# Kernel tuning notes

Measured on AMD Instinct MI355X. Metric: run time of the kernel, lower is better.

Reference implementation:

```python
import jax, jax.numpy as jnp
import numpy as np

B, S, D_MODEL, D_QK, D_VO = 4, 2048, 1024, 128, 128
NEG = -1.0e9


def setup_inputs() -> dict:
    key = jax.random.key(0)
    k1, k2, k3, k4, k5 = jax.random.split(key, 5)
    enc = jax.random.normal(k1, (B, S, D_MODEL), dtype=jnp.float32)
    # causal mask: True means masked (masked_fill), broadcast over batch
    causal = jnp.triu(jnp.ones((S, S), dtype=bool), k=1)
    mask = jnp.broadcast_to(causal, (B, S, S))
    scale = 0.02
    W_q = jax.random.normal(k2, (D_MODEL, D_QK), dtype=jnp.float32) * scale
    W_k = jax.random.normal(k3, (D_MODEL, D_QK), dtype=jnp.float32) * scale
    W_v = jax.random.normal(k4, (D_MODEL, D_VO), dtype=jnp.float32) * scale
    W_o = jax.random.normal(k5, (D_VO, D_MODEL), dtype=jnp.float32) * scale
    return {"encodings": enc, "mask": mask, "W_q": W_q, "W_k": W_k, "W_v": W_v, "W_o": W_o}


def reference(encodings, mask, W_q, W_k, W_v, W_o):
    # q,k: [B,S,d_qk]; v: [B,S,d_vo]
    q = jnp.einsum('bsd,de->bse', encodings, W_q)
    k = jnp.einsum('bsd,de->bse', encodings, W_k)
    v = jnp.einsum('bsd,de->bse', encodings, W_v)
    sims = jnp.einsum('bqe,bke->bqk', q, k) / jnp.asarray(D_QK ** 0.5, q.dtype)
    sims = jnp.where(mask, jnp.asarray(NEG, sims.dtype), sims)
    attn = jax.nn.softmax(sims, axis=-1)  # [B,S,S]
    scores = jnp.einsum('bqk,bke->bqe', attn, v)  # [B,S,d_vo]
    return jnp.einsum('bse,ed->bsd', scores, W_o)  # [B,S,d_model]
```

## Files before the change

kernel.cpp:

```cpp
#include <hip/hip_runtime.h>
#include <hip/hip_bf16.h>
#include <stdint.h>

typedef __attribute__((ext_vector_type(8))) short short8;
typedef __attribute__((ext_vector_type(4))) float floatx4;

using bf16 = __hip_bfloat16;

#define SCALE_L2 0.12751793359133147f

__device__ inline unsigned short f2b(float f) {
    bf16 h = __float2bfloat16(f);
    return *(unsigned short*)&h;
}
__device__ inline float b2f(unsigned short u) {
    union { unsigned int i; float f; } v;
    v.i = ((unsigned int)u) << 16;
    return v.f;
}

__device__ __forceinline__ void gll16(const bf16* g, bf16* l) {
    __builtin_amdgcn_global_load_lds((__attribute__((address_space(1))) void*)g,
                                     (__attribute__((address_space(3))) void*)l,
                                     16, 0, 0);
}

__global__ __launch_bounds__(256) void prep_w(const float* __restrict__ Wq,
                                              const float* __restrict__ Wk,
                                              const float* __restrict__ Wv,
                                              const float* __restrict__ Wo,
                                              bf16* __restrict__ Wqkvt,
                                              bf16* __restrict__ Wot) {
    int idx = blockIdx.x * 256 + threadIdx.x;
    int sel = idx >> 17;
    int i = idx & 131071;
    if (sel < 3) {
        const float* W = (sel == 0) ? Wq : (sel == 1) ? Wk : Wv;
        int r = i >> 7, c = i & 127;
        Wqkvt[(size_t)(sel * 128 + c) * 1024 + r] = __float2bfloat16(W[i]);
    } else {
        int r = i >> 10, c = i & 1023;
        Wot[(size_t)c * 128 + r] = __float2bfloat16(Wo[i]);
    }
}

__global__ __launch_bounds__(256) void gemm_qkv(const float* __restrict__ enc,
                                                const bf16* __restrict__ Bt,
                                                bf16* __restrict__ Qb,
                                                bf16* __restrict__ Kb,
                                                bf16* __restrict__ Vtb) {
    __shared__ __align__(16) bf16 As[32 * 32];
    __shared__ __align__(16) bf16 Bs[128 * 32];

    const int tid = threadIdx.x;
    const int m0 = blockIdx.x * 32;
    const int nsel = blockIdx.y;
    const int brow0 = nsel * 128;
    const int w = tid >> 6, lane = tid & 63;
    const int wr = (w >> 1) * 16, wc = (w & 1) * 64;
    const int quad = lane >> 4, l16 = lane & 15;

    const int ar = tid >> 3, af = tid & 7;
    const int br = w * 16 + (lane >> 2), bk = (lane & 3) * 8;

    const float4* Arow4 = (const float4*)&enc[(size_t)(m0 + ar) * 1024];
    float4 a0 = Arow4[af];

    floatx4 acc[4];
#pragma unroll
    for (int j = 0; j < 4; j++) acc[j] = (floatx4){0.f, 0.f, 0.f, 0.f};

    for (int k0 = 0; k0 < 1024; k0 += 32) {
        __syncthreads();
        gll16(&Bt[(size_t)(brow0 + br) * 1024 + k0 + bk], &Bs[w * 512]);
        gll16(&Bt[(size_t)(brow0 + 64 + br) * 1024 + k0 + bk], &Bs[2048 + w * 512]);
        ushort4 u0;
        u0.x = f2b(a0.x); u0.y = f2b(a0.y); u0.z = f2b(a0.z); u0.w = f2b(a0.w);
        *(ushort4*)&As[ar * 32 + af * 4] = u0;
        __syncthreads();

        if (k0 + 32 < 1024)
            a0 = Arow4[((k0 + 32) >> 2) + af];

        short8 a = *(const short8*)&As[(wr + l16) * 32 + quad * 8];
        short8 bfr[4];
#pragma unroll
        for (int nt = 0; nt < 4; nt++)
            bfr[nt] = *(const short8*)&Bs[(wc + nt * 16 + l16) * 32 + quad * 8];
#pragma unroll
        for (int nt = 0; nt < 4; nt++)
            acc[nt] = __builtin_amdgcn_mfma_f32_16x16x32_bf16(a, bfr[nt], acc[nt], 0, 0, 0);
    }

#pragma unroll
    for (int nt = 0; nt < 4; nt++)
#pragma unroll
        for (int r = 0; r < 4; r++) {
            int row = m0 + wr + quad * 4 + r;
            int col = wc + nt * 16 + l16;
            bf16 h = __float2bfloat16(acc[nt][r]);
            if (nsel == 0) {
                Qb[(size_t)row * 128 + col] = h;
            } else if (nsel == 1) {
                Kb[(size_t)row * 128 + col] = h;
            } else {
                int bb = row >> 11, ss = row & 2047;
                Vtb[(size_t)bb * 262144 + (size_t)col * 2048 + ss] = h;
            }
        }
}

__global__ __launch_bounds__(256) void gemm_out(const bf16* __restrict__ A,
                                                const bf16* __restrict__ Bt,
                                                float* __restrict__ C) {
    __shared__ bf16 As[64 * 40];
    __shared__ bf16 Bs[128 * 40];

    const int tid = threadIdx.x;
    const int m0 = blockIdx.x * 64;
    const int n0 = blockIdx.y * 128;
    const int w = tid >> 6, lane = tid & 63;
    const int wm = (w >> 1) * 32, wn = (w & 1) * 64;
    const int quad = lane >> 4, l16 = lane & 15;

    const int ra = tid >> 2, ca = (tid & 3) * 8;
    const int rb0 = tid >> 2, rb1 = (tid + 256) >> 2;

    floatx4 acc[2][4];
#pragma unroll
    for (int i = 0; i < 2; i++)
#pragma unroll
        for (int j = 0; j < 4; j++) acc[i][j] = (floatx4){0.f, 0.f, 0.f, 0.f};

    int4 pa  = *(const int4*)&A[(size_t)(m0 + ra) * 128 + ca];
    int4 pb0 = *(const int4*)&Bt[(size_t)(n0 + rb0) * 128 + ca];
    int4 pb1 = *(const int4*)&Bt[(size_t)(n0 + rb1) * 128 + ca];

    for (int k0 = 0; k0 < 128; k0 += 32) {
        __syncthreads();
        *(int4*)&As[ra * 40 + ca] = pa;
        *(int4*)&Bs[rb0 * 40 + ca] = pb0;
        *(int4*)&Bs[rb1 * 40 + ca] = pb1;
        __syncthreads();

        if (k0 + 32 < 128) {
            pa  = *(const int4*)&A[(size_t)(m0 + ra) * 128 + k0 + 32 + ca];
            pb0 = *(const int4*)&Bt[(size_t)(n0 + rb0) * 128 + k0 + 32 + ca];
            pb1 = *(const int4*)&Bt[(size_t)(n0 + rb1) * 128 + k0 + 32 + ca];
        }

        short8 a[2], b[4];
#pragma unroll
        for (int mt = 0; mt < 2; mt++)
            a[mt] = *(const short8*)&As[(wm + mt * 16 + l16) * 40 + quad * 8];
#pragma unroll
        for (int nt = 0; nt < 4; nt++)
            b[nt] = *(const short8*)&Bs[(wn + nt * 16 + l16) * 40 + quad * 8];
#pragma unroll
        for (int mt = 0; mt < 2; mt++)
#pragma unroll
            for (int nt = 0; nt < 4; nt++)
                acc[mt][nt] = __builtin_amdgcn_mfma_f32_16x16x32_bf16(a[mt], b[nt], acc[mt][nt], 0, 0, 0);
    }

#pragma unroll
    for (int mt = 0; mt < 2; mt++)
#pragma unroll
        for (int nt = 0; nt < 4; nt++)
#pragma unroll
            for (int r = 0; r < 4; r++) {
                int row = m0 + wm + mt * 16 + quad * 4 + r;
                int col = n0 + wn + nt * 16 + l16;
                C[(size_t)row * 1024 + col] = acc[mt][nt][r];
            }
}

__global__ __launch_bounds__(256) void flash_split(const bf16* __restrict__ Q,
                                                   const bf16* __restrict__ K,
                                                   const bf16* __restrict__ Vt,
                                                   bf16* __restrict__ Opb,
                                                   float2* __restrict__ Ml) {
    __shared__ __align__(16) char smem[74752];

    const int tid = threadIdx.x;
    const int x = blockIdx.x;
    const int b = x / 272;
    const int id = x - b * 272;
    int qt = (int)__builtin_amdgcn_sqrtf(4.0f * (float)id + 1.0f) - 1;
    if (qt < 0) qt = 0;
    while (((qt + 2) * (qt + 2)) / 4 <= id) qt++;
    while (((qt + 1) * (qt + 1)) / 4 > id) qt--;
    const int c = id - ((qt + 1) * (qt + 1)) / 4;
    const int q0 = qt * 64;
    const int start = 2 * c;
    const int end = min(start + 2, qt + 1);

    const int w = tid >> 6, lane = tid & 63;
    const int quad = lane >> 4, l16 = lane & 15;
    bf16* myP = (bf16*)(smem + 65536) + w * 1152;

    const int krow = w * 4 + (lane >> 4);
    const int kcb  = (lane & 15) * 16;
    const int vrow = w * 8 + (lane >> 3);
    const int vcb  = (lane & 7) * 16;
    const int ksw  = (l16 & 7) << 4;

    const int qrow = q0 + w * 16 + l16;
    const bf16* Qrow = &Q[((size_t)b * 2048 + qrow) * 128];
    short8 qf[4];
#pragma unroll
    for (int k4 = 0; k4 < 4; k4++)
        qf[k4] = *(const short8*)&Qrow[k4 * 32 + quad * 8];

    float m_run = -1.0e30f, l_run = 0.f;
    floatx4 o[8];
#pragma unroll
    for (int d = 0; d < 8; d++) o[d] = (floatx4){0.f, 0.f, 0.f, 0.f};

#pragma unroll 1
    for (int t = 0; t < 2; t++) {
        if (start + t >= end) break;
        const int kt = start + t;
        char* base = smem + t * 32768;
#pragma unroll
        for (int i = 0; i < 4; i++) {
            int row = i * 16 + krow;
            int cbs = kcb ^ ((row & 7) << 4);
            gll16(&K[((size_t)b * 2048 + kt * 64 + row) * 128 + (cbs >> 1)],
                  (bf16*)(base + i * 4096 + w * 1024));
        }
#pragma unroll
        for (int i = 0; i < 4; i++) {
            int row = i * 32 + vrow;
            int cbs = vcb ^ ((row & 7) << 4);
            gll16(&Vt[(size_t)b * 262144 + (size_t)row * 2048 + kt * 64 + (cbs >> 1)],
                  (bf16*)(base + 16384 + i * 4096 + w * 1024));
        }
    }
    __syncthreads();

    for (int kt = start; kt < end; kt++) {
        const char* Kb = smem + ((kt - start) & 1) * 32768;
        const char* Vb = Kb + 16384;

        floatx4 s_acc[4];
#pragma unroll
        for (int nt = 0; nt < 4; nt++) {
            s_acc[nt] = (floatx4){0.f, 0.f, 0.f, 0.f};
#pragma unroll
            for (int k4 = 0; k4 < 4; k4++) {
                short8 kf = *(const short8*)(Kb +
                              (nt * 16 + l16) * 256 + ((k4 * 64 + quad * 16) ^ ksw));
                s_acc[nt] = __builtin_amdgcn_mfma_f32_16x16x32_bf16(kf, qf[k4], s_acc[nt], 0, 0, 0);
            }
        }

        float sv[4][4];
#pragma unroll
        for (int nt = 0; nt < 4; nt++)
#pragma unroll
            for (int r = 0; r < 4; r++) {
                float s = s_acc[nt][r] * SCALE_L2;
                if (kt == qt) {
                    int kcol = kt * 64 + nt * 16 + quad * 4 + r;
                    if (kcol > qrow) s = -1.0e9f;
                }
                sv[nt][r] = s;
            }

        float t0 = fmaxf(fmaxf(sv[0][0], sv[0][1]), fmaxf(sv[0][2], sv[0][3]));
        float t1 = fmaxf(fmaxf(sv[1][0], sv[1][1]), fmaxf(sv[1][2], sv[1][3]));
        float t2 = fmaxf(fmaxf(sv[2][0], sv[2][1]), fmaxf(sv[2][2], sv[2][3]));
        float t3 = fmaxf(fmaxf(sv[3][0], sv[3][1]), fmaxf(sv[3][2], sv[3][3]));
        float tmax = fmaxf(fmaxf(t0, t1), fmaxf(t2, t3));
        tmax = fmaxf(tmax, __shfl_xor(tmax, 16));
        tmax = fmaxf(tmax, __shfl_xor(tmax, 32));

        float mnew = fmaxf(m_run, tmax);
        float alpha = exp2f(m_run - mnew);
        m_run = mnew;

        float rsum = 0.f;
#pragma unroll
        for (int nt = 0; nt < 4; nt++)
#pragma unroll
            for (int r = 0; r < 4; r++) {
                float p = exp2f(sv[nt][r] - mnew);
                sv[nt][r] = p;
                rsum += p;
            }
        rsum += __shfl_xor(rsum, 16);
        rsum += __shfl_xor(rsum, 32);
        l_run = l_run * alpha + rsum;

#pragma unroll
        for (int nt = 0; nt < 4; nt++) {
            ushort4 pk;
            pk.x = f2b(sv[nt][0]); pk.y = f2b(sv[nt][1]);
            pk.z = f2b(sv[nt][2]); pk.w = f2b(sv[nt][3]);
            *(ushort4*)&myP[l16 * 72 + nt * 16 + quad * 4] = pk;
        }

#pragma unroll
        for (int d = 0; d < 8; d++) {
            o[d][0] *= alpha; o[d][1] *= alpha; o[d][2] *= alpha; o[d][3] *= alpha;
        }

        short8 pf[2];
#pragma unroll
        for (int k2 = 0; k2 < 2; k2++)
            pf[k2] = *(const short8*)&myP[l16 * 72 + k2 * 32 + quad * 8];
#pragma unroll
        for (int d = 0; d < 8; d++)
#pragma unroll
            for (int k2 = 0; k2 < 2; k2++) {
                short8 vf = *(const short8*)(Vb +
                              (d * 16 + l16) * 128 + ((k2 * 64 + quad * 16) ^ ksw));
                o[d] = __builtin_amdgcn_mfma_f32_16x16x32_bf16(vf, pf[k2], o[d], 0, 0, 0);
            }
    }

    __syncthreads();
    bf16* myO = (bf16*)(smem + w * 4352);
#pragma unroll
    for (int d = 0; d < 8; d++) {
        ushort4 pk;
        pk.x = f2b(o[d][0]); pk.y = f2b(o[d][1]);
        pk.z = f2b(o[d][2]); pk.w = f2b(o[d][3]);
        *(ushort4*)&myO[l16 * 136 + d * 16 + quad * 4] = pk;
    }
    const int er = lane >> 2;
    const int ec = lane & 3;
    const size_t orow = ((size_t)x * 64 + w * 16 + er) * 128;
#pragma unroll
    for (int p = 0; p < 4; p++) {
        int ce = (p * 4 + ec) * 8;
        short8 t = *(const short8*)&myO[er * 136 + ce];
        *(short8*)&Opb[orow + ce] = t;
    }
    if (lane < 16) Ml[(size_t)x * 64 + w * 16 + l16] = make_float2(m_run, l_run);
}

__global__ __launch_bounds__(256) void flash_merge(const bf16* __restrict__ Opb,
                                                   const float2* __restrict__ Ml,
                                                   bf16* __restrict__ Sc) {
    int idx = blockIdx.x * 256 + threadIdx.x;
    int row = idx >> 5, dg = (idx & 31) * 4;
    int b = row >> 11, s = row & 2047;
    int qt = s >> 6, rl = s & 63;
    int nc = (qt >> 1) + 1;
    int id0 = b * 272 + ((qt + 1) * (qt + 1)) / 4;

    float M = -1.0e30f;
    for (int j = 0; j < nc; j++)
        M = fmaxf(M, Ml[(size_t)(id0 + j) * 64 + rl].x);

    float L = 0.f;
    float a0 = 0.f, a1 = 0.f, a2 = 0.f, a3 = 0.f;
    for (int j = 0; j < nc; j++) {
        float2 t = Ml[(size_t)(id0 + j) * 64 + rl];
        float wj = exp2f(t.x - M);
        L += t.y * wj;
        ushort4 p = *(const ushort4*)&Opb[((size_t)(id0 + j) * 64 + rl) * 128 + dg];
        a0 += wj * b2f(p.x); a1 += wj * b2f(p.y);
        a2 += wj * b2f(p.z); a3 += wj * b2f(p.w);
    }
    float inv = 1.0f / L;
    ushort4 o;
    o.x = f2b(a0 * inv); o.y = f2b(a1 * inv);
    o.z = f2b(a2 * inv); o.w = f2b(a3 * inv);
    *(ushort4*)&Sc[(size_t)row * 128 + dg] = o;
}

extern "C" void kernel_launch(void* const* d_in, const int* in_sizes, int n_in,
                              void* d_out, int out_size, void* d_ws, size_t ws_size,
                              hipStream_t stream) {
    const float* enc = (const float*)d_in[0];
    const float* Wq = (const float*)d_in[2];
    const float* Wk = (const float*)d_in[3];
    const float* Wv = (const float*)d_in[4];
    const float* Wo = (const float*)d_in[5];
    float* out = (float*)d_out;

    const size_t MB = 1024 * 1024;
    char* ws = (char*)d_ws;
    bf16*   Qb    = (bf16*)(ws);
    bf16*   Kb    = (bf16*)(ws + 2 * MB);
    bf16*   Vtb   = (bf16*)(ws + 4 * MB);
    bf16*   Scb   = (bf16*)(ws + 6 * MB);
    bf16*   Wqkvt = (bf16*)(ws + 8 * MB);
    bf16*   Wot   = (bf16*)(ws + 8 * MB + 768 * 1024);
    float2* Ml    = (float2*)(ws + 9 * MB);
    bf16*   Opb   = (bf16*)(ws + 10 * MB);

    prep_w<<<2048, dim3(256), 0, stream>>>(Wq, Wk, Wv, Wo, Wqkvt, Wot);

    gemm_qkv<<<dim3(256, 3), dim3(256), 0, stream>>>(enc, Wqkvt, Qb, Kb, Vtb);

    flash_split<<<1088, dim3(256), 0, stream>>>(Qb, Kb, Vtb, Opb, Ml);
    flash_merge<<<1024, dim3(256), 0, stream>>>(Opb, Ml, Scb);

    gemm_out<<<dim3(128, 8), dim3(256), 0, stream>>>(Scb, Wot, out);
}
```

Before: 190.0 us.

## Use 128-row query tiles with 512-thread blocks and single-buffered KV

Enlarges the flash-attention query tile from 64 to 128 rows by launching 512-thread blocks (8 waves), so each K/V tile loaded into shared memory is reused by twice as many query rows. The work split becomes triangular over 128-row tiles, with 136 blocks per batch, and the merge kernel's indexing is updated to match. KV staging drops from double-buffered prefetch to a single buffer that is reloaded after each tile between two barriers, which shrinks LDS use but exposes load latency with no overlap.

```diff
diff --git a/kernel.cpp b/kernel.cpp
--- a/kernel.cpp
+++ b/kernel.cpp
@@ -175,29 +175,31 @@
             }
 }
 
-__global__ __launch_bounds__(256) void flash_split(const bf16* __restrict__ Q,
+__global__ __launch_bounds__(512) void flash_split(const bf16* __restrict__ Q,
                                                    const bf16* __restrict__ K,
                                                    const bf16* __restrict__ Vt,
                                                    bf16* __restrict__ Opb,
                                                    float2* __restrict__ Ml) {
-    __shared__ __align__(16) char smem[74752];
+    __shared__ __align__(16) char smem[51200];
 
     const int tid = threadIdx.x;
     const int x = blockIdx.x;
-    const int b = x / 272;
-    const int id = x - b * 272;
-    int qt = (int)__builtin_amdgcn_sqrtf(4.0f * (float)id + 1.0f) - 1;
+    const int b = x / 136;
+    const int id = x - b * 136;
+    int qt = (int)((__builtin_amdgcn_sqrtf(8.0f * (float)id + 1.0f) - 1.0f) * 0.5f);
     if (qt < 0) qt = 0;
-    while (((qt + 2) * (qt + 2)) / 4 <= id) qt++;
-    while (((qt + 1) * (qt + 1)) / 4 > id) qt--;
-    const int c = id - ((qt + 1) * (qt + 1)) / 4;
-    const int q0 = qt * 64;
+    while ((qt + 1) * (qt + 2) / 2 <= id) qt++;
+    while (qt * (qt + 1) / 2 > id) qt--;
+    const int c = id - qt * (qt + 1) / 2;
+    const int q0 = qt * 128;
     const int start = 2 * c;
-    const int end = min(start + 2, qt + 1);
+    const int end = min(start + 2, 2 * qt + 2);
 
     const int w = tid >> 6, lane = tid & 63;
     const int quad = lane >> 4, l16 = lane & 15;
-    bf16* myP = (bf16*)(smem + 65536) + w * 1152;
+    bf16* Ks = (bf16*)smem;
+    bf16* Vs = (bf16*)(smem + 16384);
+    bf16* myP = (bf16*)(smem + 32768) + w * 1152;
 
     const int krow = w * 4 + (lane >> 4);
     const int kcb  = (lane & 15) * 16;
@@ -217,51 +219,46 @@
 #pragma unroll
     for (int d = 0; d < 8; d++) o[d] = (floatx4){0.f, 0.f, 0.f, 0.f};
 
-#pragma unroll 1
-    for (int t = 0; t < 2; t++) {
-        if (start + t >= end) break;
-        const int kt = start + t;
-        char* base = smem + t * 32768;
-#pragma unroll
-        for (int i = 0; i < 4; i++) {
-            int row = i * 16 + krow;
+    {
+        const int kt = start;
+#pragma unroll
+        for (int i = 0; i < 2; i++) {
+            int row = i * 32 + krow;
             int cbs = kcb ^ ((row & 7) << 4);
             gll16(&K[((size_t)b * 2048 + kt * 64 + row) * 128 + (cbs >> 1)],
-                  (bf16*)(base + i * 4096 + w * 1024));
-        }
-#pragma unroll
-        for (int i = 0; i < 4; i++) {
-            int row = i * 32 + vrow;
+                  &Ks[i * 4096 + w * 512]);
+        }
+#pragma unroll
+        for (int i = 0; i < 2; i++) {
+            int row = i * 64 + vrow;
             int cbs = vcb ^ ((row & 7) << 4);
             gll16(&Vt[(size_t)b * 262144 + (size_t)row * 2048 + kt * 64 + (cbs >> 1)],
-                  (bf16*)(base + 16384 + i * 4096 + w * 1024));
+                  &Vs[i * 4096 + w * 512]);
         }
     }
     __syncthreads();
 
     for (int kt = start; kt < end; kt++) {
-        const char* Kb = smem + ((kt - start) & 1) * 32768;
-        const char* Vb = Kb + 16384;
-
         floatx4 s_acc[4];
 #pragma unroll
         for (int nt = 0; nt < 4; nt++) {
             s_acc[nt] = (floatx4){0.f, 0.f, 0.f, 0.f};
 #pragma unroll
             for (int k4 = 0; k4 < 4; k4++) {
-                short8 kf = *(const short8*)(Kb +
+                short8 kf = *(const short8*)((const char*)Ks +
                               (nt * 16 + l16) * 256 + ((k4 * 64 + quad * 16) ^ ksw));
                 s_acc[nt] = __builtin_amdgcn_mfma_f32_16x16x32_bf16(kf, qf[k4], s_acc[nt], 0, 0, 0);
             }
         }
 
         float sv[4][4];
+        const bool diag = (kt >= 2 * qt);
 #pragma unroll
         for (int nt = 0; nt < 4; nt++)
 #pragma unroll
             for (int r = 0; r < 4; r++) {
                 float s = s_acc[nt][r] * SCALE_L2;
-                if (kt == qt) {
+                if (diag) {
                     int kcol = kt * 64 + nt * 16 + quad * 4 + r;
                     if (kcol > qrow) s = -1.0e9f;
                 }
@@ -314,10 +311,30 @@
         for (int d = 0; d < 8; d++)
 #pragma unroll
             for (int k2 = 0; k2 < 2; k2++) {
-                short8 vf = *(const short8*)(Vb +
+                short8 vf = *(const short8*)((const char*)Vs +
                               (d * 16 + l16) * 128 + ((k2 * 64 + quad * 16) ^ ksw));
                 o[d] = __builtin_amdgcn_mfma_f32_16x16x32_bf16(vf, pf[k2], o[d], 0, 0, 0);
             }
+
+        if (kt + 1 < end) {
+            __syncthreads();
+            const int nk = kt + 1;
+#pragma unroll
+            for (int i = 0; i < 2; i++) {
+                int row = i * 32 + krow;
+                int cbs = kcb ^ ((row & 7) << 4);
+                gll16(&K[((size_t)b * 2048 + nk * 64 + row) * 128 + (cbs >> 1)],
+                      &Ks[i * 4096 + w * 512]);
+            }
+#pragma unroll
+            for (int i = 0; i < 2; i++) {
+                int row = i * 64 + vrow;
+                int cbs = vcb ^ ((row & 7) << 4);
+                gll16(&Vt[(size_t)b * 262144 + (size_t)row * 2048 + nk * 64 + (cbs >> 1)],
+                      &Vs[i * 4096 + w * 512]);
+            }
+            __syncthreads();
+        }
     }
 
     __syncthreads();
@@ -331,14 +348,14 @@
     }
     const int er = lane >> 2;
     const int ec = lane & 3;
-    const size_t orow = ((size_t)x * 64 + w * 16 + er) * 128;
+    const size_t orow = ((size_t)x * 128 + w * 16 + er) * 128;
 #pragma unroll
     for (int p = 0; p < 4; p++) {
         int ce = (p * 4 + ec) * 8;
         short8 t = *(const short8*)&myO[er * 136 + ce];
         *(short8*)&Opb[orow + ce] = t;
     }
-    if (lane < 16) Ml[(size_t)x * 64 + w * 16 + l16] = make_float2(m_run, l_run);
+    if (lane < 16) Ml[(size_t)x * 128 + w * 16 + l16] = make_float2(m_run, l_run);
 }
 
 __global__ __launch_bounds__(256) void flash_merge(const bf16* __restrict__ Opb,
@@ -347,21 +364,21 @@
     int idx = blockIdx.x * 256 + threadIdx.x;
     int row = idx >> 5, dg = (idx & 31) * 4;
     int b = row >> 11, s = row & 2047;
-    int qt = s >> 6, rl = s & 63;
-    int nc = (qt >> 1) + 1;
-    int id0 = b * 272 + ((qt + 1) * (qt + 1)) / 4;
+    int qt = s >> 7, rl = s & 127;
+    int nc = qt + 1;
+    int id0 = b * 136 + qt * (qt + 1) / 2;
 
     float M = -1.0e30f;
     for (int j = 0; j < nc; j++)
-        M = fmaxf(M, Ml[(size_t)(id0 + j) * 64 + rl].x);
+        M = fmaxf(M, Ml[(size_t)(id0 + j) * 128 + rl].x);
 
     float L = 0.f;
     float a0 = 0.f, a1 = 0.f, a2 = 0.f, a3 = 0.f;
     for (int j = 0; j < nc; j++) {
-        float2 t = Ml[(size_t)(id0 + j) * 64 + rl];
+        float2 t = Ml[(size_t)(id0 + j) * 128 + rl];
         float wj = exp2f(t.x - M);
         L += t.y * wj;
-        ushort4 p = *(const ushort4*)&Opb[((size_t)(id0 + j) * 64 + rl) * 128 + dg];
+        ushort4 p = *(const ushort4*)&Opb[((size_t)(id0 + j) * 128 + rl) * 128 + dg];
         a0 += wj * b2f(p.x); a1 += wj * b2f(p.y);
         a2 += wj * b2f(p.z); a3 += wj * b2f(p.w);
     }
@@ -397,7 +414,7 @@
 
     gemm_qkv<<<dim3(256, 3), dim3(256), 0, stream>>>(enc, Wqkvt, Qb, Kb, Vtb);
 
-    flash_split<<<1088, dim3(256), 0, stream>>>(Qb, Kb, Vtb, Opb, Ml);
+    flash_split<<<544, dim3(512), 0, stream>>>(Qb, Kb, Vtb, Opb, Ml);
     flash_merge<<<1024, dim3(256), 0, stream>>>(Opb, Ml, Scb);
 
     gemm_out<<<dim3(128, 8), dim3(256), 0, stream>>>(Scb, Wot, out);
```

Result: no change. 190.4 us (+0.2%).
